# Kernel tuning notes

Hardware: AMD Instinct MI355X
Metric: run time of the kernel (lower is better)

The kernel has to match this reference:

```python
import jax, jax.numpy as jnp
import numpy as np

N = 100000      # num nodes (== num hyperedges, since hyperedge ids are node indices)
H = 128         # hidden_dim
E = 800000      # incidence pairs (node, hyperedge)
NEG_SLOPE = 0.2 # PyG HypergraphConv leaky_relu negative_slope


def prelu(x, a):
    return jnp.where(x >= 0, x, a * x)


def segment_softmax(logits, seg, num_segments):
    m = jax.ops.segment_max(logits, seg, num_segments=num_segments)
    m = jnp.where(jnp.isfinite(m), m, 0.0)  # empty segments -> 0
    e = jnp.exp(logits - m[seg])
    s = jax.ops.segment_sum(e, seg, num_segments=num_segments)
    return e / (s[seg] + 1e-16)


def hconv(x, W, att, b, row, col):
    """PyG HypergraphConv, use_attention=True, attention_mode='node', heads=1,
    hyperedge_attr = x (hyperedge ids are node indices; legacy PyG behavior).
    row = node index of incidence, col = hyperedge index of incidence."""
    xw = x @ W  # [N, H]
    a_i, a_j = att[:H], att[H:]
    # alpha = leaky_relu(<[x_i||x_j], att>) ; computed without materializing the concat
    logits = jax.nn.leaky_relu((xw @ a_i)[row] + (xw @ a_j)[col], NEG_SLOPE)
    alpha = segment_softmax(logits, col, N)  # attention_mode='node' -> softmax over hyperedge
    # degrees: D via node (row), B via hyperedge (col); unit hyperedge weights
    ones = jnp.ones_like(alpha)
    D = jax.ops.segment_sum(ones, row, num_segments=N)
    D_inv = jnp.where(D > 0, 1.0 / D, 0.0)
    B = jax.ops.segment_sum(ones, col, num_segments=N)
    B_inv = jnp.where(B > 0, 1.0 / B, 0.0)
    # node -> hyperedge: e_f[e] = B_inv[e] * sum_{(v,e)} alpha * xw[v]
    edge_feat = B_inv[:, None] * jax.ops.segment_sum(alpha[:, None] * xw[row], col, num_segments=N)
    # hyperedge -> node: out[v] = D_inv[v] * sum_{(v,e)} alpha * e_f[e]
    out = D_inv[:, None] * jax.ops.segment_sum(alpha[:, None] * edge_feat[col], row, num_segments=N)
    return out + b


def setup_inputs() -> dict:
    key = jax.random.key(0)
    ks = jax.random.split(key, 8)
    x = jax.random.normal(ks[0], (N, H), dtype=jnp.float32)
    hyperedge_index = jax.random.randint(ks[1], (2, E), 0, N, dtype=jnp.int64)
    kaiming = np.sqrt(2.0 / H)
    glorot = np.sqrt(6.0 / (2 * H + 1))
    W1 = jax.random.normal(ks[2], (H, H), dtype=jnp.float32) * kaiming
    W2 = jax.random.normal(ks[3], (H, H), dtype=jnp.float32) * kaiming
    att1 = jax.random.uniform(ks[4], (2 * H,), dtype=jnp.float32, minval=-glorot, maxval=glorot)
    att2 = jax.random.uniform(ks[5], (2 * H,), dtype=jnp.float32, minval=-glorot, maxval=glorot)
    b1 = jnp.zeros((H,), dtype=jnp.float32)
    b2 = jnp.zeros((H,), dtype=jnp.float32)
    prelu_a = jnp.array(0.25, dtype=jnp.float32)
    return {"x": x, "hyperedge_index": hyperedge_index, "W1": W1, "att1": att1,
            "b1": b1, "W2": W2, "att2": att2, "b2": b2, "prelu_a": prelu_a}


def reference(x, hyperedge_index, W1, att1, b1, W2, att2, b2, prelu_a):
    row, col = hyperedge_index[0], hyperedge_index[1]
    out1 = prelu(hconv(x, W1, att1, b1, row, col), prelu_a)
    out1 = hconv(out1, W2, att2, b2, row, col) + x  # residual
    return prelu(out1, prelu_a)
```

## Files before the change

kernel.cpp:

```cpp
#include <hip/hip_runtime.h>
#include <hip/hip_bf16.h>
#include <math.h>

#define HD 128
#define NEG_SLOPE 0.2f

typedef __attribute__((ext_vector_type(8))) short bf16x8;
typedef __attribute__((ext_vector_type(4))) float f32x4;

static __device__ __forceinline__ unsigned short bfc(float f) {
    __hip_bfloat16 h = __float2bfloat16(f);
    return *(unsigned short*)&h;
}
static __device__ __forceinline__ float bflo(unsigned u) { return __uint_as_float(u << 16); }
static __device__ __forceinline__ float bfhi(unsigned u) { return __uint_as_float(u & 0xFFFF0000u); }


__global__ void k_hist(const int* __restrict__ row, const int* __restrict__ col,
                       int* __restrict__ hc, int* __restrict__ hr,
                       int* __restrict__ ocol, int* __restrict__ orow, int E) {
    int e = blockIdx.x * blockDim.x + threadIdx.x;
    if (e < E) {
        ocol[e] = atomicAdd(&hc[col[e]], 1);
        orow[e] = atomicAdd(&hr[row[e]], 1);
    }
}

__device__ __forceinline__ int blk_exscan(int v, int t, int* ws) {
    int inc = v;
    #pragma unroll
    for (int o = 1; o < 64; o <<= 1) {
        int u = __shfl_up(inc, o);
        if ((t & 63) >= o) inc += u;
    }
    int w = t >> 6;
    if ((t & 63) == 63) ws[w] = inc;
    __syncthreads();
    int off = 0;
    for (int i = 0; i < w; ++i) off += ws[i];
    return off + inc - v;
}

__global__ void k_scan1(const int* __restrict__ h, int* __restrict__ part, int n2) {
    __shared__ int ws[4];
    int t = threadIdx.x;
    int i = blockIdx.x * 256 + t;
    int v = (i < n2) ? h[i] : 0;
    #pragma unroll
    for (int o = 32; o > 0; o >>= 1) v += __shfl_down(v, o);
    if ((t & 63) == 0) ws[t >> 6] = v;
    __syncthreads();
    if (t == 0) part[blockIdx.x] = ws[0] + ws[1] + ws[2] + ws[3];
}

__global__ __launch_bounds__(1024) void k_scan2(int* __restrict__ part, int nb) {
    __shared__ int ws[16];
    int t = threadIdx.x;
    int v = (t < nb) ? part[t] : 0;
    int e = blk_exscan(v, t, ws);
    if (t < nb) part[t] = e;
}

__global__ void k_scan3(const int* __restrict__ h, const int* __restrict__ part,
                        int* __restrict__ cptr, int* __restrict__ rptr,
                        int n1, int n2, int E) {
    __shared__ int ws[4];
    int t = threadIdx.x;
    int i = blockIdx.x * 256 + t;
    int v = (i < n2) ? h[i] : 0;
    int e = blk_exscan(v, t, ws);
    if (i <= n2) {
        int val = part[blockIdx.x] + e;
        if (i <= n1) cptr[i] = val;
        if (i >= n1) rptr[i - n1] = val - E;
    }
}

__global__ void k_fill(const int* __restrict__ row, const int* __restrict__ col,
                       const int* __restrict__ cptr, const int* __restrict__ rptr,
                       const int* __restrict__ ocol, const int* __restrict__ orow,
                       int* __restrict__ crows, int2* __restrict__ rpack, int E) {
    int e = blockIdx.x * blockDim.x + threadIdx.x;
    if (e >= E) return;
    int r = row[e], c = col[e];
    int cp = cptr[c] + ocol[e];
    int rp = rptr[r] + orow[e];
    crows[cp] = r;
    rpack[rp] = make_int2(c, cp);
}


__global__ __launch_bounds__(256) void k_gemm(const float* __restrict__ in,
                                              const float* __restrict__ W,
                                              const float* __restrict__ att,
                                              unsigned short* __restrict__ xwb,
                                              float* __restrict__ sI,
                                              float* __restrict__ sJ,
                                              int nrows, int ntiles) {
    __shared__ unsigned short xb[64 * 128];
    __shared__ unsigned short Wt[128 * 128];
    const int t = threadIdx.x;
    const int l = t & 63;
    const int w = t >> 6;
    const int m16 = l & 15;
    const int q4  = l >> 4;

    float ai8[8], aj8[8];
    #pragma unroll
    for (int ct = 0; ct < 8; ++ct) {
        ai8[ct] = att[(ct << 4) + m16];
        aj8[ct] = att[HD + (ct << 4) + m16];
    }

    {
        int col = t >> 1;
        #pragma unroll
        for (int i = 0; i < 8; ++i) {
            int kc = ((t & 1) << 3) + i;
            unsigned short tmp[8];
            #pragma unroll
            for (int j = 0; j < 8; ++j)
                tmp[j] = bfc(W[((kc << 3) + j) * HD + col]);
            *(bf16x8*)&Wt[col * 128 + ((kc ^ (col & 7)) << 3)] = *(bf16x8*)tmp;
        }
    }

    for (int tile = blockIdx.x; tile < ntiles; tile += gridDim.x) {
        const int r0 = tile << 6;
        __syncthreads();
        {
            int row = t >> 2;
            int gr = r0 + row;
            #pragma unroll
            for (int i = 0; i < 4; ++i) {
                int kc = ((t & 3) << 2) + i;
                unsigned short tmp[8];
                if (gr < nrows) {
                    float4 f0 = *(const float4*)&in[(size_t)gr * HD + (kc << 3)];
                    float4 f1 = *(const float4*)&in[(size_t)gr * HD + (kc << 3) + 4];
                    tmp[0] = bfc(f0.x); tmp[1] = bfc(f0.y); tmp[2] = bfc(f0.z); tmp[3] = bfc(f0.w);
                    tmp[4] = bfc(f1.x); tmp[5] = bfc(f1.y); tmp[6] = bfc(f1.z); tmp[7] = bfc(f1.w);
                } else {
                    #pragma unroll
                    for (int j = 0; j < 8; ++j) tmp[j] = 0;
                }
                *(bf16x8*)&xb[row * 128 + ((kc ^ (row & 7)) << 3)] = *(bf16x8*)tmp;
            }
        }
        __syncthreads();

        f32x4 acc[8];
        #pragma unroll
        for (int ct = 0; ct < 8; ++ct) acc[ct] = (f32x4){0.f, 0.f, 0.f, 0.f};

        const int arow = (w << 4) + m16;
        #pragma unroll
        for (int ks = 0; ks < 4; ++ks) {
            int akc = (ks << 2) + q4;
            bf16x8 av = *(const bf16x8*)&xb[arow * 128 + ((akc ^ (arow & 7)) << 3)];
            #pragma unroll
            for (int ct = 0; ct < 8; ++ct) {
                int col = (ct << 4) + m16;
                bf16x8 bv = *(const bf16x8*)&Wt[col * 128 + ((akc ^ (col & 7)) << 3)];
                acc[ct] = __builtin_amdgcn_mfma_f32_16x16x32_bf16(av, bv, acc[ct], 0, 0, 0);
            }
        }

        const int rbase = r0 + (w << 4) + (q4 << 2);
        #pragma unroll
        for (int ct = 0; ct < 8; ++ct) {
            int col = (ct << 4) + m16;
            #pragma unroll
            for (int i = 0; i < 4; ++i) {
                int gr = rbase + i;
                if (gr < nrows) xwb[(size_t)gr * HD + col] = bfc(acc[ct][i]);
            }
        }
        float p[4] = {0.f, 0.f, 0.f, 0.f}, qv[4] = {0.f, 0.f, 0.f, 0.f};
        #pragma unroll
        for (int ct = 0; ct < 8; ++ct)
            #pragma unroll
            for (int i = 0; i < 4; ++i) {
                p[i]  += acc[ct][i] * ai8[ct];
                qv[i] += acc[ct][i] * aj8[ct];
            }
        #pragma unroll
        for (int o = 1; o <= 8; o <<= 1) {
            #pragma unroll
            for (int i = 0; i < 4; ++i) {
                p[i]  += __shfl_xor(p[i], o);
                qv[i] += __shfl_xor(qv[i], o);
            }
        }
        if (m16 == 0) {
            #pragma unroll
            for (int i = 0; i < 4; ++i) {
                int gr = rbase + i;
                if (gr < nrows) { sI[gr] = p[i]; sJ[gr] = qv[i]; }
            }
        }
    }
}


__global__ __launch_bounds__(256) void k_efsm(const float* __restrict__ sI,
                                              const float* __restrict__ sJ,
                                              const int* __restrict__ cptr,
                                              const int* __restrict__ crows,
                                              float* __restrict__ alpha,
                                              const unsigned short* __restrict__ xwb,
                                              unsigned short* __restrict__ efb, int n) {
    int c = blockIdx.x * 4 + (threadIdx.x >> 6);
    if (c >= n) return;
    int l = threadIdx.x & 63;
    int p0 = cptr[c], p1 = cptr[c + 1];
    int deg = p1 - p0;
    size_t eoff = (size_t)c * HD + 2 * l;
    if (deg == 0) {
        *(unsigned*)&efb[eoff] = 0u;
        return;
    }
    float sj = sJ[c];
    float ax = 0.f, ay = 0.f;
    if (deg <= 64) {
        int p = p0 + l;
        int r = 0;
        float lg = -1e30f;
        if (l < deg) {
            r = crows[p];
            float v = sI[r] + sj;
            lg = v >= 0.f ? v : NEG_SLOPE * v;
        }
        float mm = lg;
        #pragma unroll
        for (int o = 32; o > 0; o >>= 1) mm = fmaxf(mm, __shfl_xor(mm, o));
        float ev = (l < deg) ? __expf(lg - mm) : 0.f;
        float ss = ev;
        #pragma unroll
        for (int o = 32; o > 0; o >>= 1) ss += __shfl_xor(ss, o);
        float a = ev / (ss + 1e-16f);
        if (l < deg) alpha[p] = a;
        int k = 0;
        for (; k + 4 <= deg; k += 4) {
            float a0 = __shfl(a, k),     a1 = __shfl(a, k + 1);
            float a2 = __shfl(a, k + 2), a3 = __shfl(a, k + 3);
            int   r0 = __shfl(r, k),     r1 = __shfl(r, k + 1);
            int   r2 = __shfl(r, k + 2), r3 = __shfl(r, k + 3);
            unsigned u0 = *(const unsigned*)&xwb[(size_t)r0 * HD + 2 * l];
            unsigned u1 = *(const unsigned*)&xwb[(size_t)r1 * HD + 2 * l];
            unsigned u2 = *(const unsigned*)&xwb[(size_t)r2 * HD + 2 * l];
            unsigned u3 = *(const unsigned*)&xwb[(size_t)r3 * HD + 2 * l];
            ax += a0 * bflo(u0) + a1 * bflo(u1) + a2 * bflo(u2) + a3 * bflo(u3);
            ay += a0 * bfhi(u0) + a1 * bfhi(u1) + a2 * bfhi(u2) + a3 * bfhi(u3);
        }
        for (; k < deg; ++k) {
            float av = __shfl(a, k);
            int   rv = __shfl(r, k);
            unsigned u = *(const unsigned*)&xwb[(size_t)rv * HD + 2 * l];
            ax += av * bflo(u); ay += av * bfhi(u);
        }
    } else {
        float m = -1e30f, s = 0.f;
        for (int base = p0; base < p1; base += 64) {
            int p = base + l;
            float lg = -1e30f;
            if (p < p1) {
                float v = sI[crows[p]] + sj;
                lg = v >= 0.f ? v : NEG_SLOPE * v;
            }
            float mm = lg;
            #pragma unroll
            for (int o = 32; o > 0; o >>= 1) mm = fmaxf(mm, __shfl_xor(mm, o));
            float newm = fmaxf(m, mm);
            float ev = (p < p1) ? __expf(lg - newm) : 0.f;
            float ss = ev;
            #pragma unroll
            for (int o = 32; o > 0; o >>= 1) ss += __shfl_xor(ss, o);
            s = s * __expf(m - newm) + ss;
            m = newm;
        }
        float inv = 1.f / (s + 1e-16f);
        for (int base = p0; base < p1; base += 64) {
            int p = base + l;
            float a = 0.f; int r = 0;
            if (p < p1) {
                r = crows[p];
                float v = sI[r] + sj;
                v = v >= 0.f ? v : NEG_SLOPE * v;
                a = __expf(v - m) * inv;
                alpha[p] = a;
            }
            int cnt = min(64, p1 - base);
            for (int k = 0; k < cnt; ++k) {
                float av = __shfl(a, k);
                int   rv = __shfl(r, k);
                unsigned u = *(const unsigned*)&xwb[(size_t)rv * HD + 2 * l];
                ax += av * bflo(u); ay += av * bfhi(u);
            }
        }
    }
    float binv = 1.f / (float)deg;
    unsigned outw = ((unsigned)bfc(ax * binv)) | (((unsigned)bfc(ay * binv)) << 16);
    *(unsigned*)&efb[eoff] = outw;
}


__global__ __launch_bounds__(256) void k_out(const int* __restrict__ rptr,
                                             const int2* __restrict__ rpack,
                                             const float* __restrict__ alpha,
                                             const unsigned short* __restrict__ efb,
                                             const float* __restrict__ bias,
                                             const float* __restrict__ resid,
                                             const float* __restrict__ pa,
                                             float* __restrict__ out, int n) {
    int nd = blockIdx.x * 4 + (threadIdx.x >> 6);
    if (nd >= n) return;
    int l = threadIdx.x & 63;
    int p0 = rptr[nd], p1 = rptr[nd + 1];
    float ax = 0.f, ay = 0.f;
    for (int base = p0; base < p1; base += 64) {
        int p = base + l;
        int cc = 0; float a = 0.f;
        if (p < p1) {
            int2 pk = rpack[p];
            cc = pk.x;
            a = alpha[pk.y];
        }
        int cnt = min(64, p1 - base);
        int k = 0;
        for (; k + 4 <= cnt; k += 4) {
            float a0 = __shfl(a, k),     a1 = __shfl(a, k + 1);
            float a2 = __shfl(a, k + 2), a3 = __shfl(a, k + 3);
            int   c0 = __shfl(cc, k),     c1 = __shfl(cc, k + 1);
            int   c2 = __shfl(cc, k + 2), c3 = __shfl(cc, k + 3);
            unsigned u0 = *(const unsigned*)&efb[(size_t)c0 * HD + 2 * l];
            unsigned u1 = *(const unsigned*)&efb[(size_t)c1 * HD + 2 * l];
            unsigned u2 = *(const unsigned*)&efb[(size_t)c2 * HD + 2 * l];
            unsigned u3 = *(const unsigned*)&efb[(size_t)c3 * HD + 2 * l];
            ax += a0 * bflo(u0) + a1 * bflo(u1) + a2 * bflo(u2) + a3 * bflo(u3);
            ay += a0 * bfhi(u0) + a1 * bfhi(u1) + a2 * bfhi(u2) + a3 * bfhi(u3);
        }
        for (; k < cnt; ++k) {
            float av = __shfl(a, k);
            int   cv = __shfl(cc, k);
            unsigned u = *(const unsigned*)&efb[(size_t)cv * HD + 2 * l];
            ax += av * bflo(u); ay += av * bfhi(u);
        }
    }
    float dinv = (p1 > p0) ? 1.f / (float)(p1 - p0) : 0.f;
    int h = 2 * l;
    float vx = dinv * ax + bias[h];
    float vy = dinv * ay + bias[h + 1];
    size_t idx = (size_t)nd * HD + h;
    if (resid) { vx += resid[idx]; vy += resid[idx + 1]; }
    float s = pa[0];
    vx = vx >= 0.f ? vx : s * vx;
    vy = vy >= 0.f ? vy : s * vy;
    out[idx] = vx; out[idx + 1] = vy;
}


extern "C" void kernel_launch(void* const* d_in, const int* in_sizes, int n_in,
                              void* d_out, int out_size, void* d_ws, size_t ws_size,
                              hipStream_t stream) {
    const float* x    = (const float*)d_in[0];
    const int*   hei  = (const int*)d_in[1];
    const float* W1   = (const float*)d_in[2];
    const float* att1 = (const float*)d_in[3];
    const float* b1   = (const float*)d_in[4];
    const float* W2   = (const float*)d_in[5];
    const float* att2 = (const float*)d_in[6];
    const float* b2   = (const float*)d_in[7];
    const float* pa   = (const float*)d_in[8];

    const int NH = in_sizes[0];
    const int Nn = NH / HD;
    const int E  = in_sizes[1] / 2;
    const int* row = hei;
    const int* col = hei + E;
    float* out = (float*)d_out;

    char* ws = (char*)d_ws;
    unsigned short* xwb = (unsigned short*)ws;         ws += (size_t)NH * 2;
    unsigned short* efb = (unsigned short*)ws;         ws += (size_t)NH * 2;
    float* alpha   = (float*)ws;                       ws += (size_t)E * 4;
    int*   crows   = (int*)ws;                         ws += (size_t)E * 4;
    int2*  rpack   = (int2*)ws;                        ws += (size_t)E * 8;
    int*   cptr    = (int*)ws;                         ws += (size_t)(Nn + 1) * 4;
    int*   rptr    = (int*)ws;                         ws += (size_t)(Nn + 1) * 4;
    int*   hists   = (int*)ws;                         ws += (size_t)2 * Nn * 4;
    int*   part    = (int*)ws;                         ws += 1024 * 4;
    float* sI      = (float*)ws;                       ws += (size_t)Nn * 4;
    float* sJ      = (float*)ws;                       ws += (size_t)Nn * 4;
    int* hc = hists, *hr = hists + Nn;
    int* ocol = (int*)alpha;
    int* orow = (int*)d_out;

    const int TB = 256;
    dim3 blk(TB);
    dim3 gE((E + TB - 1) / TB);
    dim3 gW4((Nn + 3) / 4);
    const int n2 = 2 * Nn;
    const int nb = (n2 + 1 + 255) / 256;
    const int ntiles = (Nn + 63) >> 6;
    int gg = 768;
    if (gg > ntiles) gg = ntiles;
    dim3 gGemm(gg);

    hipMemsetAsync(hists, 0, (size_t)n2 * 4, stream);
    k_hist<<<gE, blk, 0, stream>>>(row, col, hc, hr, ocol, orow, E);
    k_scan1<<<nb, blk, 0, stream>>>(hists, part, n2);
    k_scan2<<<1, 1024, 0, stream>>>(part, nb);
    k_scan3<<<nb, blk, 0, stream>>>(hists, part, cptr, rptr, Nn, n2, E);
    k_fill<<<gE, blk, 0, stream>>>(row, col, cptr, rptr, ocol, orow, crows, rpack, E);

    k_gemm<<<gGemm, blk, 0, stream>>>(x, W1, att1, xwb, sI, sJ, Nn, ntiles);
    k_efsm<<<gW4, blk, 0, stream>>>(sI, sJ, cptr, crows, alpha, xwb, efb, Nn);
    k_out<<<gW4, blk, 0, stream>>>(rptr, rpack, alpha, efb, b1, nullptr, pa, out, Nn);

    k_gemm<<<gGemm, blk, 0, stream>>>(out, W2, att2, xwb, sI, sJ, Nn, ntiles);
    k_efsm<<<gW4, blk, 0, stream>>>(sI, sJ, cptr, crows, alpha, xwb, efb, Nn);
    k_out<<<gW4, blk, 0, stream>>>(rptr, rpack, alpha, efb, b2, x, pa, out, Nn);
}
```

Before: 369.3 us.

## Store layer-1 output in bf16, pre-convert weights, compact incidence packing

```diff
diff --git a/kernel.cpp b/kernel.cpp
--- a/kernel.cpp
+++ b/kernel.cpp
@@ -79,19 +79,37 @@
 __global__ void k_fill(const int* __restrict__ row, const int* __restrict__ col,
                        const int* __restrict__ cptr, const int* __restrict__ rptr,
                        const int* __restrict__ ocol, const int* __restrict__ orow,
-                       int* __restrict__ crows, int2* __restrict__ rpack, int E) {
+                       int* __restrict__ crows, unsigned* __restrict__ rpack, int E) {
     int e = blockIdx.x * blockDim.x + threadIdx.x;
     if (e >= E) return;
     int r = row[e], c = col[e];
-    int cp = cptr[c] + ocol[e];
+    int oc = ocol[e];
+    int cp = cptr[c] + oc;
     int rp = rptr[r] + orow[e];
     crows[cp] = r;
-    rpack[rp] = make_int2(c, cp);
-}
-
-
-__global__ __launch_bounds__(256) void k_gemm(const float* __restrict__ in,
-                                              const float* __restrict__ W,
+    rpack[rp] = ((unsigned)c << 8) | (unsigned)(oc & 255);
+}
+
+
+__global__ void k_prep(const float* __restrict__ W1, const float* __restrict__ W2,
+                       unsigned short* __restrict__ WbT1, unsigned short* __restrict__ WbT2) {
+    int idx = blockIdx.x * 256 + threadIdx.x;
+    const float* W = (idx < 2048) ? W1 : W2;
+    unsigned short* D = (idx < 2048) ? WbT1 : WbT2;
+    int rem = idx & 2047;
+    int col = rem >> 4;
+    int kc  = rem & 15;
+    unsigned short tmp[8];
+    #pragma unroll
+    for (int j = 0; j < 8; ++j)
+        tmp[j] = bfc(W[((kc << 3) + j) * HD + col]);
+    *(bf16x8*)&D[col * 128 + ((kc ^ (col & 7)) << 3)] = *(bf16x8*)tmp;
+}
+
+
+template <bool IN_BF>
+__global__ __launch_bounds__(256) void k_gemm(const void* __restrict__ inp,
+                                              const unsigned short* __restrict__ WbT,
                                               const float* __restrict__ att,
                                               unsigned short* __restrict__ xwb,
                                               float* __restrict__ sI,
@@ -112,17 +130,10 @@
         aj8[ct] = att[HD + (ct << 4) + m16];
     }
 
-    {
-        int col = t >> 1;
-        #pragma unroll
-        for (int i = 0; i < 8; ++i) {
-            int kc = ((t & 1) << 3) + i;
-            unsigned short tmp[8];
-            #pragma unroll
-            for (int j = 0; j < 8; ++j)
-                tmp[j] = bfc(W[((kc << 3) + j) * HD + col]);
-            *(bf16x8*)&Wt[col * 128 + ((kc ^ (col & 7)) << 3)] = *(bf16x8*)tmp;
-        }
+    #pragma unroll
+    for (int i = 0; i < 8; ++i) {
+        int off = (t << 3) + (i << 11);
+        *(bf16x8*)&Wt[off] = *(const bf16x8*)&WbT[off];
     }
 
     for (int tile = blockIdx.x; tile < ntiles; tile += gridDim.x) {
@@ -134,17 +145,24 @@
             #pragma unroll
             for (int i = 0; i < 4; ++i) {
                 int kc = ((t & 3) << 2) + i;
-                unsigned short tmp[8];
+                bf16x8 v;
                 if (gr < nrows) {
-                    float4 f0 = *(const float4*)&in[(size_t)gr * HD + (kc << 3)];
-                    float4 f1 = *(const float4*)&in[(size_t)gr * HD + (kc << 3) + 4];
-                    tmp[0] = bfc(f0.x); tmp[1] = bfc(f0.y); tmp[2] = bfc(f0.z); tmp[3] = bfc(f0.w);
-                    tmp[4] = bfc(f1.x); tmp[5] = bfc(f1.y); tmp[6] = bfc(f1.z); tmp[7] = bfc(f1.w);
+                    if (IN_BF) {
+                        v = *(const bf16x8*)&((const unsigned short*)inp)[(size_t)gr * HD + (kc << 3)];
+                    } else {
+                        const float* in = (const float*)inp;
+                        float4 f0 = *(const float4*)&in[(size_t)gr * HD + (kc << 3)];
+                        float4 f1 = *(const float4*)&in[(size_t)gr * HD + (kc << 3) + 4];
+                        unsigned short tmp[8];
+                        tmp[0] = bfc(f0.x); tmp[1] = bfc(f0.y); tmp[2] = bfc(f0.z); tmp[3] = bfc(f0.w);
+                        tmp[4] = bfc(f1.x); tmp[5] = bfc(f1.y); tmp[6] = bfc(f1.z); tmp[7] = bfc(f1.w);
+                        v = *(bf16x8*)tmp;
+                    }
                 } else {
-                    #pragma unroll
-                    for (int j = 0; j < 8; ++j) tmp[j] = 0;
+                    unsigned short z[8] = {0,0,0,0,0,0,0,0};
+                    v = *(bf16x8*)z;
                 }
-                *(bf16x8*)&xb[row * 128 + ((kc ^ (row & 7)) << 3)] = *(bf16x8*)tmp;
+                *(bf16x8*)&xb[row * 128 + ((kc ^ (row & 7)) << 3)] = v;
             }
         }
         __syncthreads();
@@ -305,14 +323,16 @@
 }
 
 
+template <bool LAST>
 __global__ __launch_bounds__(256) void k_out(const int* __restrict__ rptr,
-                                             const int2* __restrict__ rpack,
+                                             const unsigned* __restrict__ rpack,
+                                             const int* __restrict__ cptr,
                                              const float* __restrict__ alpha,
                                              const unsigned short* __restrict__ efb,
                                              const float* __restrict__ bias,
                                              const float* __restrict__ resid,
                                              const float* __restrict__ pa,
-                                             float* __restrict__ out, int n) {
+                                             void* __restrict__ outp, int n) {
     int nd = blockIdx.x * 4 + (threadIdx.x >> 6);
     if (nd >= n) return;
     int l = threadIdx.x & 63;
@@ -322,9 +342,9 @@
         int p = base + l;
         int cc = 0; float a = 0.f;
         if (p < p1) {
-            int2 pk = rpack[p];
-            cc = pk.x;
-            a = alpha[pk.y];
+            unsigned pk = rpack[p];
+            cc = (int)(pk >> 8);
+            a = alpha[cptr[cc] + (int)(pk & 255u)];
         }
         int cnt = min(64, p1 - base);
         int k = 0;
@@ -352,11 +372,17 @@
     float vx = dinv * ax + bias[h];
     float vy = dinv * ay + bias[h + 1];
     size_t idx = (size_t)nd * HD + h;
-    if (resid) { vx += resid[idx]; vy += resid[idx + 1]; }
+    if (LAST) { vx += resid[idx]; vy += resid[idx + 1]; }
     float s = pa[0];
     vx = vx >= 0.f ? vx : s * vx;
     vy = vy >= 0.f ? vy : s * vy;
-    out[idx] = vx; out[idx + 1] = vy;
+    if (LAST) {
+        float* out = (float*)outp;
+        out[idx] = vx; out[idx + 1] = vy;
+    } else {
+        unsigned short* ob = (unsigned short*)outp;
+        *(unsigned*)&ob[idx] = ((unsigned)bfc(vx)) | (((unsigned)bfc(vy)) << 16);
+    }
 }
 
 
@@ -381,17 +407,20 @@
     float* out = (float*)d_out;
 
     char* ws = (char*)d_ws;
-    unsigned short* xwb = (unsigned short*)ws;         ws += (size_t)NH * 2;
-    unsigned short* efb = (unsigned short*)ws;         ws += (size_t)NH * 2;
+    unsigned short* xwb  = (unsigned short*)ws;        ws += (size_t)NH * 2;
+    unsigned short* efb  = (unsigned short*)ws;        ws += (size_t)NH * 2;
+    unsigned short* h1b  = (unsigned short*)ws;        ws += (size_t)NH * 2;
     float* alpha   = (float*)ws;                       ws += (size_t)E * 4;
     int*   crows   = (int*)ws;                         ws += (size_t)E * 4;
-    int2*  rpack   = (int2*)ws;                        ws += (size_t)E * 8;
+    unsigned* rpack = (unsigned*)ws;                   ws += (size_t)E * 4;
     int*   cptr    = (int*)ws;                         ws += (size_t)(Nn + 1) * 4;
     int*   rptr    = (int*)ws;                         ws += (size_t)(Nn + 1) * 4;
     int*   hists   = (int*)ws;                         ws += (size_t)2 * Nn * 4;
     int*   part    = (int*)ws;                         ws += 1024 * 4;
     float* sI      = (float*)ws;                       ws += (size_t)Nn * 4;
     float* sJ      = (float*)ws;                       ws += (size_t)Nn * 4;
+    unsigned short* WbT1 = (unsigned short*)ws;        ws += (size_t)HD * HD * 2;
+    unsigned short* WbT2 = (unsigned short*)ws;        ws += (size_t)HD * HD * 2;
     int* hc = hists, *hr = hists + Nn;
     int* ocol = (int*)alpha;
     int* orow = (int*)d_out;
@@ -407,6 +436,7 @@
     if (gg > ntiles) gg = ntiles;
     dim3 gGemm(gg);
 
+    k_prep<<<16, blk, 0, stream>>>(W1, W2, WbT1, WbT2);
     hipMemsetAsync(hists, 0, (size_t)n2 * 4, stream);
     k_hist<<<gE, blk, 0, stream>>>(row, col, hc, hr, ocol, orow, E);
     k_scan1<<<nb, blk, 0, stream>>>(hists, part, n2);
@@ -414,11 +444,11 @@
     k_scan3<<<nb, blk, 0, stream>>>(hists, part, cptr, rptr, Nn, n2, E);
     k_fill<<<gE, blk, 0, stream>>>(row, col, cptr, rptr, ocol, orow, crows, rpack, E);
 
-    k_gemm<<<gGemm, blk, 0, stream>>>(x, W1, att1, xwb, sI, sJ, Nn, ntiles);
+    k_gemm<false><<<gGemm, blk, 0, stream>>>(x, WbT1, att1, xwb, sI, sJ, Nn, ntiles);
     k_efsm<<<gW4, blk, 0, stream>>>(sI, sJ, cptr, crows, alpha, xwb, efb, Nn);
-    k_out<<<gW4, blk, 0, stream>>>(rptr, rpack, alpha, efb, b1, nullptr, pa, out, Nn);
-
-    k_gemm<<<gGemm, blk, 0, stream>>>(out, W2, att2, xwb, sI, sJ, Nn, ntiles);
+    k_out<false><<<gW4, blk, 0, stream>>>(rptr, rpack, cptr, alpha, efb, b1, nullptr, pa, h1b, Nn);
+
+    k_gemm<true><<<gGemm, blk, 0, stream>>>(h1b, WbT2, att2, xwb, sI, sJ, Nn, ntiles);
     k_efsm<<<gW4, blk, 0, stream>>>(sI, sJ, cptr, crows, alpha, xwb, efb, Nn);
-    k_out<<<gW4, blk, 0, stream>>>(rptr, rpack, alpha, efb, b2, x, pa, out, Nn);
-}
+    k_out<true><<<gW4, blk, 0, stream>>>(rptr, rpack, cptr, alpha, efb, b2, x, pa, out, Nn);
+}
```

Result: faster. 357.5 us (-3.2%).
